# Kernel tuning notes

Hardware: AMD Instinct MI355X
Metric: run time of the kernel (lower is better)

## Reference

```python
import jax, jax.numpy as jnp
import numpy as np

D_MODEL = 1024
HEADS = 16
D_K = D_MODEL // HEADS
D_FF = 4096
EPS = 1e-5


def _layernorm(x, gamma, beta):
    mu = jnp.mean(x, axis=-1, keepdims=True)
    var = jnp.var(x, axis=-1, keepdims=True)
    return (x - mu) * jax.lax.rsqrt(var + EPS) * gamma + beta


def setup_inputs() -> dict:
    key = jax.random.key(0)
    ks = jax.random.split(key, 8)
    s = 0.02
    return {
        "x": jax.random.normal(ks[0], (4, 2048, D_MODEL), dtype=jnp.float32),
        "wq": jax.random.normal(ks[1], (D_MODEL, D_MODEL), dtype=jnp.float32) * s,
        "wk": jax.random.normal(ks[2], (D_MODEL, D_MODEL), dtype=jnp.float32) * s,
        "wv": jax.random.normal(ks[3], (D_MODEL, D_MODEL), dtype=jnp.float32) * s,
        "wo": jax.random.normal(ks[4], (D_MODEL, D_MODEL), dtype=jnp.float32) * s,
        "w1": jax.random.normal(ks[5], (D_MODEL, D_FF), dtype=jnp.float32) * s,
        "b1": jnp.zeros((D_FF,), dtype=jnp.float32),
        "w2": jax.random.normal(ks[6], (D_FF, D_MODEL), dtype=jnp.float32) * s,
        "b2": jnp.zeros((D_MODEL,), dtype=jnp.float32),
        "g1": jnp.ones((D_MODEL,), dtype=jnp.float32),
        "be1": jnp.zeros((D_MODEL,), dtype=jnp.float32),
        "g2": jnp.ones((D_MODEL,), dtype=jnp.float32),
        "be2": jnp.zeros((D_MODEL,), dtype=jnp.float32),
    }


def reference(x, wq, wk, wv, wo, w1, b1, w2, b2, g1, be1, g2, be2):
    B, S, D = x.shape
    # --- multi-head self-attention (dropout = identity at eval) ---
    q = (x @ wq).reshape(B, S, HEADS, D_K).transpose(0, 2, 1, 3)  # [B,H,S,dk]
    k = (x @ wk).reshape(B, S, HEADS, D_K).transpose(0, 2, 1, 3)
    v = (x @ wv).reshape(B, S, HEADS, D_K).transpose(0, 2, 1, 3)
    scores = jnp.einsum("bhqd,bhkd->bhqk", q, k) / jnp.sqrt(jnp.float32(D_K))
    attn = jax.nn.softmax(scores, axis=-1)
    ctx = jnp.einsum("bhqk,bhkd->bhqd", attn, v)
    ctx = ctx.transpose(0, 2, 1, 3).reshape(B, S, D)
    attn_out = ctx @ wo
    # --- add & norm 1 ---
    h = _layernorm(x + attn_out, g1, be1)
    # --- FFN ---
    ffn = jax.nn.relu(h @ w1 + b1) @ w2 + b2
    # --- add & norm 2 ---
    return _layernorm(h + ffn, g2, be2)
```

## Files before the change

### kernel.cpp

```cpp
#include <hip/hip_runtime.h>
#include <hip/hip_bf16.h>


typedef float  floatx2  __attribute__((ext_vector_type(2)));
typedef float  floatx4  __attribute__((ext_vector_type(4)));
typedef float  floatx16 __attribute__((ext_vector_type(16)));
typedef short  shortx8  __attribute__((ext_vector_type(8)));
typedef short  shortx4  __attribute__((ext_vector_type(4)));
typedef int    intx4    __attribute__((ext_vector_type(4)));
typedef unsigned uintx2 __attribute__((ext_vector_type(2)));

__device__ __forceinline__ short f2bs(float f) {
    union { float f; unsigned u; } a; a.f = f;
    unsigned r = a.u + 0x7fffu + ((a.u >> 16) & 1u);
    return (short)(r >> 16);
}

__device__ __forceinline__ float fexp2(float x) {
#if __has_builtin(__builtin_amdgcn_exp2f)
    return __builtin_amdgcn_exp2f(x);
#else
    return __expf(0.6931471805599453f * x);
#endif
}

__device__ __forceinline__ void lane32swap(unsigned& a, unsigned& b) {
#if __has_builtin(__builtin_amdgcn_permlane32_swap)
    uintx2 r = __builtin_amdgcn_permlane32_swap(a, b, false, false);
    a = r[0]; b = r[1];
#else
    int hl = (threadIdx.x & 63) >> 5;
    unsigned ta = (unsigned)__shfl_xor((int)a, 32);
    unsigned tb = (unsigned)__shfl_xor((int)b, 32);
    unsigned na = hl ? tb : a;
    unsigned nb = hl ? b : ta;
    a = na; b = nb;
#endif
}

__device__ __forceinline__ void gload16(const short* g, short* l) {
    __builtin_amdgcn_global_load_lds(
        (const __attribute__((address_space(1))) void*)g,
        (__attribute__((address_space(3))) void*)l,
        16, 0, 0);
}

#define WAITV(n) asm volatile("s_waitcnt vmcnt(" #n ")" ::: "memory")
#define FENCE    asm volatile("" ::: "memory")

__device__ __forceinline__ void trans_tile(const float* __restrict__ in,
                                           short* __restrict__ out,
                                           int N, int K, int k0, int n0,
                                           short (*t)[68]) {
    const int tid = threadIdx.x;
    const int r = tid >> 4, c4 = (tid & 15) * 4;
#pragma unroll
    for (int i = 0; i < 4; ++i) {
        int k = r + i * 16;
        floatx4 v = *(const floatx4*)(in + (size_t)(k0 + k) * N + n0 + c4);
        shortx4 s;
#pragma unroll
        for (int j = 0; j < 4; ++j) s[j] = f2bs(v[j]);
        *(shortx4*)(&t[k][c4]) = s;
    }
    __syncthreads();
#pragma unroll
    for (int i = 0; i < 4; ++i) {
        int n = r + i * 16;
        shortx4 s;
#pragma unroll
        for (int j = 0; j < 4; ++j) s[j] = t[c4 + j][n];
        *(shortx4*)(out + (size_t)(n0 + n) * K + k0 + c4) = s;
    }
}

__global__ __launch_bounds__(256) void prep_kernel(
    const float* __restrict__ wq, const float* __restrict__ wk,
    const float* __restrict__ wv, const float* __restrict__ wo,
    const float* __restrict__ w1, const float* __restrict__ w2,
    const float* __restrict__ x,
    short* wqt, short* wkt, short* wvt, short* wot,
    short* w1t, short* w2t, short* xb)
{
    __shared__ __align__(16) short t[64][68];
    const int bid = blockIdx.x;
    if (bid < 1024) {
        const int widx = bid >> 8, local = bid & 255;
        const float* in = widx == 0 ? wq : widx == 1 ? wk : widx == 2 ? wv : wo;
        short* out = widx == 0 ? wqt : widx == 1 ? wkt : widx == 2 ? wvt : wot;
        trans_tile(in, out, 1024, 1024, (local & 15) * 64, (local >> 4) * 64, t);
    } else if (bid < 2048) {
        const int local = bid - 1024;
        trans_tile(w1, w1t, 4096, 1024, (local & 15) * 64, (local >> 4) * 64, t);
    } else if (bid < 3072) {
        const int local = bid - 2048;
        trans_tile(w2, w2t, 1024, 4096, (local & 63) * 64, (local >> 6) * 64, t);
    } else {
        const int local = bid - 3072;
#pragma unroll
        for (int j = 0; j < 4; ++j) {
            int i = local * 1024 + j * 256 + threadIdx.x;
            floatx4 v = *(const floatx4*)(x + (size_t)i * 4);
            shortx4 o;
            o[0] = f2bs(v[0]); o[1] = f2bs(v[1]); o[2] = f2bs(v[2]); o[3] = f2bs(v[3]);
            *(shortx4*)(xb + (size_t)i * 4) = o;
        }
    }
}

template<int EPI, int BN>
__global__ __launch_bounds__(512, 2) void gemm256(
    const short* __restrict__ A, const short* __restrict__ Bt, const int K, const int N,
    short* __restrict__ outb, float* __restrict__ outf,
    const float* __restrict__ bias, const float* __restrict__ resf)
{
    constexpr int BUFSZ = 16384 + BN * 64;
    constexpr int NF = BN / 64;
    constexpr int NBUF = (BN == 128) ? 3 : 2;
    __shared__ __align__(16) short Ls[NBUF * BUFSZ];
    const int tid = threadIdx.x;
    const int w = tid >> 6, lane = tid & 63;
    const int quad = lane >> 4, l16 = lane & 15;
    const int wm = w >> 2, wn = w & 3;
    const int hsw = blockIdx.x + blockIdx.y * gridDim.x;
    const int vv = hsw >> 3;
    const int by = (hsw & 7) * 4 + (vv & 3);
    const int bx = vv >> 2;

    const int srow = w * 16 + (lane >> 3);
    const int uc0 = ((lane & 7) ^ ((lane >> 4) & 7)) * 8;
    const int uc1 = ((lane & 7) ^ (((lane >> 4) + 4) & 7)) * 8;
    const short* aS0 = A  + (size_t)(by * 256 + srow) * K + uc0;
    const short* aS1 = A  + (size_t)(by * 256 + srow + 8) * K + uc1;
    const short* bS0 = Bt + (size_t)(bx * BN + srow) * K + uc0;
    const short* bS1 = Bt + (size_t)(bx * BN + srow + 8) * K + uc1;
    const size_t hK = (size_t)128 * K;
    const int wsl = w * 1024;

    const int rswz = (l16 >> 1) & 7;
    const int ru0 = (quad ^ rswz) * 8;
    const int ru1 = ((4 + quad) ^ rswz) * 8;
    const int aRd = (wm * 64 + l16) * 64;
    const int bRd = (wn * 32 + l16) * 64;

    floatx4 acc[8][NF] = {};
    shortx8 af[4][2], blo[2][2], bhi[2][2];

#define S_A0(buf, kc) { short* p = Ls + (buf) * BUFSZ + wsl;         gload16(aS0 + (kc), p);      gload16(aS1 + (kc), p + 512);      FENCE; }
#define S_A1(buf, kc) { short* p = Ls + (buf) * BUFSZ + 8192 + wsl;  gload16(aS0 + hK + (kc), p); gload16(aS1 + hK + (kc), p + 512); FENCE; }
#define S_B0(buf, kc) { short* p = Ls + (buf) * BUFSZ + 16384 + wsl; gload16(bS0 + (kc), p);      gload16(bS1 + (kc), p + 512);      FENCE; }
#define S_B1(buf, kc) { short* p = Ls + (buf) * BUFSZ + 24576 + wsl; gload16(bS0 + hK + (kc), p); gload16(bS1 + hK + (kc), p + 512); FENCE; }
#define MF(a, b, c) c = __builtin_amdgcn_mfma_f32_16x16x32_bf16(a, b, c, 0, 0, 0)

#define RD_ALO(Ab) {                                                      \
_Pragma("unroll")                                                         \
        for (int mf = 0; mf < 4; ++mf) {                                  \
            af[mf][0] = *(const shortx8*)((Ab) + aRd + mf * 1024 + ru0);  \
            af[mf][1] = *(const shortx8*)((Ab) + aRd + mf * 1024 + ru1);  \
        } }
#define RD_AHI(Ab) {                                                      \
_Pragma("unroll")                                                         \
        for (int mf = 0; mf < 4; ++mf) {                                  \
            af[mf][0] = *(const shortx8*)((Ab) + aRd + 8192 + mf * 1024 + ru0); \
            af[mf][1] = *(const shortx8*)((Ab) + aRd + 8192 + mf * 1024 + ru1); \
        } }
#define RD_BLO(Bb) {                                                      \
_Pragma("unroll")                                                         \
        for (int nf = 0; nf < 2; ++nf) {                                  \
            blo[nf][0] = *(const shortx8*)((Bb) + bRd + nf * 1024 + ru0); \
            blo[nf][1] = *(const shortx8*)((Bb) + bRd + nf * 1024 + ru1); \
        } }
#define MFMA_LO { __builtin_amdgcn_s_setprio(1);                          \
_Pragma("unroll")                                                         \
        for (int mf = 0; mf < 4; ++mf)                                    \
_Pragma("unroll")                                                         \
            for (int nf = 0; nf < 2; ++nf) {                              \
                MF(af[mf][0], blo[nf][0], acc[mf][nf]);                   \
                MF(af[mf][1], blo[nf][1], acc[mf][nf]);                   \
            }                                                             \
        __builtin_amdgcn_s_setprio(0); }
#define MFMA_HI { __builtin_amdgcn_s_setprio(1);                          \
_Pragma("unroll")                                                         \
        for (int mf = 0; mf < 4; ++mf)                                    \
_Pragma("unroll")                                                         \
            for (int nf = 0; nf < 2; ++nf) {                              \
                MF(af[mf][0], blo[nf][0], acc[4 + mf][nf]);               \
                MF(af[mf][1], blo[nf][1], acc[4 + mf][nf]);               \
            }                                                             \
        __builtin_amdgcn_s_setprio(0); }

    const int NT = K >> 6;

    if constexpr (BN == 256) {
        S_A0(0, 0) S_B0(0, 0) S_B1(0, 0) S_A1(0, 0)
        for (int t = 0; t < NT - 1; ++t) {
            const int rb = t & 1, wbuf = rb ^ 1, kc = (t + 1) * 64;
            const short* Ab = Ls + rb * BUFSZ;
            const short* Bb = Ab + 16384;
            WAITV(4); __builtin_amdgcn_s_barrier(); FENCE;
            RD_ALO(Ab) RD_BLO(Bb)
            S_A0(wbuf, kc)
            MFMA_LO
            WAITV(4); __builtin_amdgcn_s_barrier(); FENCE;
#pragma unroll
            for (int nf = 0; nf < 2; ++nf) {
                bhi[nf][0] = *(const shortx8*)(Bb + bRd + 8192 + nf * 1024 + ru0);
                bhi[nf][1] = *(const shortx8*)(Bb + bRd + 8192 + nf * 1024 + ru1);
            }
            S_B0(wbuf, kc)
            __builtin_amdgcn_s_setprio(1);
#pragma unroll
            for (int mf = 0; mf < 4; ++mf)
#pragma unroll
                for (int nf = 0; nf < 2; ++nf) {
                    MF(af[mf][0], bhi[nf][0], acc[mf][2 + nf]);
                    MF(af[mf][1], bhi[nf][1], acc[mf][2 + nf]);
                }
            __builtin_amdgcn_s_setprio(0);
            WAITV(4); __builtin_amdgcn_s_barrier(); FENCE;
            RD_AHI(Ab)
            S_B1(wbuf, kc)
            MFMA_HI
            S_A1(wbuf, kc)
            __builtin_amdgcn_s_setprio(1);
#pragma unroll
            for (int mf = 0; mf < 4; ++mf)
#pragma unroll
                for (int nf = 0; nf < 2; ++nf) {
                    MF(af[mf][0], bhi[nf][0], acc[4 + mf][2 + nf]);
                    MF(af[mf][1], bhi[nf][1], acc[4 + mf][2 + nf]);
                }
            __builtin_amdgcn_s_setprio(0);
        }
        {
            const int rb = (NT - 1) & 1;
            const short* Ab = Ls + rb * BUFSZ;
            const short* Bb = Ab + 16384;
            WAITV(4); __builtin_amdgcn_s_barrier(); FENCE;
            RD_ALO(Ab) RD_BLO(Bb)
            MFMA_LO
            WAITV(2); __builtin_amdgcn_s_barrier(); FENCE;
#pragma unroll
            for (int nf = 0; nf < 2; ++nf) {
                bhi[nf][0] = *(const shortx8*)(Bb + bRd + 8192 + nf * 1024 + ru0);
                bhi[nf][1] = *(const shortx8*)(Bb + bRd + 8192 + nf * 1024 + ru1);
            }
            __builtin_amdgcn_s_setprio(1);
#pragma unroll
            for (int mf = 0; mf < 4; ++mf)
#pragma unroll
                for (int nf = 0; nf < 2; ++nf) {
                    MF(af[mf][0], bhi[nf][0], acc[mf][2 + nf]);
                    MF(af[mf][1], bhi[nf][1], acc[mf][2 + nf]);
                }
            __builtin_amdgcn_s_setprio(0);
            WAITV(0); __builtin_amdgcn_s_barrier(); FENCE;
            RD_AHI(Ab)
            __builtin_amdgcn_s_setprio(1);
#pragma unroll
            for (int mf = 0; mf < 4; ++mf)
#pragma unroll
                for (int nf = 0; nf < 2; ++nf) {
                    MF(af[mf][0], blo[nf][0], acc[4 + mf][nf]);
                    MF(af[mf][1], blo[nf][1], acc[4 + mf][nf]);
                    MF(af[mf][0], bhi[nf][0], acc[4 + mf][2 + nf]);
                    MF(af[mf][1], bhi[nf][1], acc[4 + mf][2 + nf]);
                }
            __builtin_amdgcn_s_setprio(0);
        }
    } else {
        S_A0(0, 0) S_B0(0, 0) S_A1(0, 0)
        S_A0(1, 64) S_B0(1, 64) S_A1(1, 64)
        for (int t = 0; t < NT - 2; ++t) {
            const int rb = t % 3, pb = (t + 2) % 3, kc = (t + 2) * 64;
            const short* Ab = Ls + rb * BUFSZ;
            const short* Bb = Ab + 16384;
            WAITV(8); __builtin_amdgcn_s_barrier(); FENCE;
            RD_ALO(Ab) RD_BLO(Bb)
            S_A0(pb, kc)
            MFMA_LO
            WAITV(8); __builtin_amdgcn_s_barrier(); FENCE;
            RD_AHI(Ab)
            S_B0(pb, kc) S_A1(pb, kc)
            MFMA_HI
        }
        {
            const int rb = (NT - 2) % 3;
            const short* Ab = Ls + rb * BUFSZ;
            const short* Bb = Ab + 16384;
            WAITV(8); __builtin_amdgcn_s_barrier(); FENCE;
            RD_ALO(Ab) RD_BLO(Bb)
            MFMA_LO
            WAITV(6); __builtin_amdgcn_s_barrier(); FENCE;
            RD_AHI(Ab)
            MFMA_HI
        }
        {
            const int rb = (NT - 1) % 3;
            const short* Ab = Ls + rb * BUFSZ;
            const short* Bb = Ab + 16384;
            WAITV(2); __builtin_amdgcn_s_barrier(); FENCE;
            RD_ALO(Ab) RD_BLO(Bb)
            MFMA_LO
            WAITV(0); __builtin_amdgcn_s_barrier(); FENCE;
            RD_AHI(Ab)
            MFMA_HI
        }
    }

#pragma unroll
    for (int mf = 0; mf < 8; ++mf) {
        const int grow0 = by * 256 + (mf >> 2) * 128 + wm * 64 + (mf & 3) * 16 + quad * 4;
#pragma unroll
        for (int nf = 0; nf < NF; ++nf) {
            int gcol;
            if constexpr (BN == 256)
                gcol = bx * 256 + (nf >> 1) * 128 + wn * 32 + (nf & 1) * 16 + l16;
            else
                gcol = bx * 128 + wn * 32 + nf * 16 + l16;
            const floatx4 a = acc[mf][nf];
            if constexpr (EPI == 5) {
                const int slice = gcol >> 10, c = gcol & 1023;
                const int hh = c >> 6, d = c & 63;
                const int b = grow0 >> 11, s0 = grow0 & 2047;
                if (slice == 2) {
                    short* vt = outb + ((size_t)16 << 20);
                    shortx4 pkv;
#pragma unroll
                    for (int r = 0; r < 4; ++r) pkv[r] = f2bs(a[r]);
                    *(shortx4*)(vt + ((size_t)((b * 16 + hh) * 64 + d)) * 2048 + s0) = pkv;
                } else {
                    short* dst = slice ? (outb + ((size_t)8 << 20)) : outb;
                    float sc = slice ? 1.f : 0.125f * 1.4426950408889634f;
#pragma unroll
                    for (int r = 0; r < 4; ++r)
                        dst[(((size_t)(b * 16 + hh)) * 2048 + (s0 + r)) * 64 + d] =
                            f2bs(a[r] * sc);
                }
            } else if constexpr (EPI == 1) {
                const float bv = bias[gcol];
#pragma unroll
                for (int r = 0; r < 4; ++r) {
                    float v = fmaxf(a[r] + bv, 0.f);
                    outb[(size_t)(grow0 + r) * N + gcol] = f2bs(v);
                }
            } else if constexpr (EPI == 2) {
#pragma unroll
                for (int r = 0; r < 4; ++r)
                    outf[(size_t)(grow0 + r) * N + gcol] =
                        a[r] + resf[(size_t)(grow0 + r) * N + gcol];
            } else if constexpr (EPI == 3) {
                const float bv = bias[gcol];
#pragma unroll
                for (int r = 0; r < 4; ++r)
                    outf[(size_t)(grow0 + r) * N + gcol] =
                        a[r] + bv + resf[(size_t)(grow0 + r) * N + gcol];
            }
        }
    }
#undef S_A0
#undef S_A1
#undef S_B0
#undef S_B1
#undef MF
#undef RD_ALO
#undef RD_AHI
#undef RD_BLO
#undef MFMA_LO
#undef MFMA_HI
}

__global__ __launch_bounds__(256) void ln_kernel(
    const float* __restrict__ in, float* __restrict__ outf, short* __restrict__ outb,
    const float* __restrict__ g, const float* __restrict__ be, int writeB)
{
    __shared__ float red[8];
    const int row = blockIdx.x, tid = threadIdx.x;
    const float* p = in + (size_t)row * 1024;
    floatx4 v = *(const floatx4*)(p + tid * 4);
    float s = v[0] + v[1] + v[2] + v[3];
    float q = v[0] * v[0] + v[1] * v[1] + v[2] * v[2] + v[3] * v[3];
#pragma unroll
    for (int off = 32; off; off >>= 1) {
        s += __shfl_xor(s, off);
        q += __shfl_xor(q, off);
    }
    int w = tid >> 6, lane = tid & 63;
    if (lane == 0) { red[w] = s; red[4 + w] = q; }
    __syncthreads();
    s = red[0] + red[1] + red[2] + red[3];
    q = red[4] + red[5] + red[6] + red[7];
    float mean = s * (1.f / 1024.f);
    float var = q * (1.f / 1024.f) - mean * mean;
    float rs = rsqrtf(var + 1e-5f);
    floatx4 gv = *(const floatx4*)(g + tid * 4);
    floatx4 bv = *(const floatx4*)(be + tid * 4);
    floatx4 o4;
#pragma unroll
    for (int i = 0; i < 4; ++i) o4[i] = (v[i] - mean) * rs * gv[i] + bv[i];
    *(floatx4*)(outf + (size_t)row * 1024 + tid * 4) = o4;
    if (writeB) {
        shortx4 ob;
#pragma unroll
        for (int i = 0; i < 4; ++i) ob[i] = f2bs(o4[i]);
        *(shortx4*)(outb + (size_t)row * 1024 + tid * 4) = ob;
    }
}

__global__ __launch_bounds__(256, 2) void attn_kernel(
    const short* __restrict__ Q, const short* __restrict__ K,
    const short* __restrict__ Vt, short* __restrict__ ctx)
{
    __shared__ __align__(16) short Ls[18432];
    const int tid = threadIdx.x;
    const int q0 = blockIdx.x * 256, bh = blockIdx.y;
    const int w = tid >> 6, lane = tid & 63, l31 = lane & 31, hl = lane >> 5;
    const size_t sb = (size_t)bh * 2048 * 64;

    shortx8 qf[2][4];
#pragma unroll
    for (int qg = 0; qg < 2; ++qg)
#pragma unroll
        for (int ks = 0; ks < 4; ++ks)
            qf[qg][ks] = *(const shortx8*)(Q + sb + (size_t)(q0 + w * 64 + qg * 32 + l31) * 64 + ks * 16 + hl * 8);

    const int srow = w * 8 + (lane >> 3);
    const int sunit = ((lane & 7) ^ (lane >> 3)) * 8;
    const short* kSrc = K + sb + (size_t)srow * 64 + sunit;
    const short* vSrc = Vt + sb + (size_t)srow * 2048 + sunit;
    const int sdst = w * 512;

    const int kx = l31 & 7;

    floatx16 o[2][2] = {};
    floatx2 rs0A = {0.f, 0.f}, rs0B = {0.f, 0.f};
    floatx2 rs1A = {0.f, 0.f}, rs1B = {0.f, 0.f};
    const floatx16 z = {};

#define STAGE(buf, kv0) { \
    short* kb = Ls + (buf) * 8192 + sdst; \
    gload16(kSrc + (size_t)(kv0) * 64, kb); \
    gload16(kSrc + (size_t)(kv0) * 64 + 2048, kb + 2048); \
    gload16(vSrc + (kv0), kb + 4096); \
    gload16(vSrc + (kv0) + 65536, kb + 6144); \
    FENCE; }

#define LD_AK(B, mt, ks) (*(const shortx8*)((B) + ((mt) * 32 + l31) * 64 + ((((ks) * 2 + hl) ^ kx)) * 8))
#define LD_AV(B, mtd, mt, ksl) (*(const shortx8*)((B) + 4096 + ((mtd) * 32 + l31) * 64 + ((((mt) * 4 + (ksl) * 2 + hl) ^ kx)) * 8))
#define MFA(a, b, c) __builtin_amdgcn_mfma_f32_32x32x16_bf16(a, b, c, 0, 0, 0)

    STAGE(0, 0)

    for (int kt = 0; kt < 32; ++kt) {
        WAITV(0);
        __builtin_amdgcn_s_barrier();
        FENCE;
        if (kt < 31) STAGE((kt + 1) & 1, (kt + 1) * 64)
        const short* B = Ls + (kt & 1) * 8192;

#pragma unroll
        for (int mt = 0; mt < 2; ++mt) {
            shortx8 ak[4], av[2][2];
#pragma unroll
            for (int ks = 0; ks < 4; ++ks) ak[ks] = LD_AK(B, mt, ks);
#pragma unroll
            for (int ksl = 0; ksl < 2; ++ksl)
#pragma unroll
                for (int mtd = 0; mtd < 2; ++mtd) av[ksl][mtd] = LD_AV(B, mtd, mt, ksl);
            floatx16 sc0, sc1;
            __builtin_amdgcn_s_setprio(1);
            sc0 = MFA(ak[0], qf[0][0], z);
            sc0 = MFA(ak[1], qf[0][1], sc0);
            sc0 = MFA(ak[2], qf[0][2], sc0);
            sc0 = MFA(ak[3], qf[0][3], sc0);
            sc1 = MFA(ak[0], qf[1][0], z);
            sc1 = MFA(ak[1], qf[1][1], sc1);
            sc1 = MFA(ak[2], qf[1][2], sc1);
            sc1 = MFA(ak[3], qf[1][3], sc1);
            __builtin_amdgcn_s_setprio(0);
#pragma unroll
            for (int qg = 0; qg < 2; ++qg) {
                const floatx16 sc = qg ? sc1 : sc0;
                floatx2 ps2[8];
#pragma unroll
                for (int i = 0; i < 8; ++i) {
                    ps2[i][0] = fexp2(sc[2 * i]);
                    ps2[i][1] = fexp2(sc[2 * i + 1]);
                }
                if (qg == 0) {
#pragma unroll
                    for (int i = 0; i < 8; i += 2) { rs0A += ps2[i]; rs0B += ps2[i + 1]; }
                } else {
#pragma unroll
                    for (int i = 0; i < 8; i += 2) { rs1A += ps2[i]; rs1B += ps2[i + 1]; }
                }
                unsigned pk[8];
#pragma unroll
                for (int i = 0; i < 8; ++i) {
                    union { __hip_bfloat162 h; unsigned u; } cv;
                    cv.h = __float22bfloat162_rn(make_float2(ps2[i][0], ps2[i][1]));
                    pk[i] = cv.u;
                }
                lane32swap(pk[0], pk[2]);
                lane32swap(pk[1], pk[3]);
                lane32swap(pk[4], pk[6]);
                lane32swap(pk[5], pk[7]);
                __builtin_amdgcn_s_setprio(1);
#pragma unroll
                for (int ksl = 0; ksl < 2; ++ksl) {
                    union { unsigned i[4]; shortx8 s8; } fr;
                    fr.i[0] = pk[4 * ksl];     fr.i[1] = pk[4 * ksl + 1];
                    fr.i[2] = pk[4 * ksl + 2]; fr.i[3] = pk[4 * ksl + 3];
#pragma unroll
                    for (int mtd = 0; mtd < 2; ++mtd)
                        o[qg][mtd] = MFA(av[ksl][mtd], fr.s8, o[qg][mtd]);
                }
                __builtin_amdgcn_s_setprio(0);
            }
        }
    }
#undef STAGE
#undef LD_AK
#undef LD_AV
#undef MFA

    float inv0, inv1;
    {
        float r0 = rs0A[0] + rs0A[1] + rs0B[0] + rs0B[1];
        float t0 = r0 + __shfl_xor(r0, 32);
        inv0 = 1.f / t0;
        float r1 = rs1A[0] + rs1A[1] + rs1B[0] + rs1B[1];
        float t1 = r1 + __shfl_xor(r1, 32);
        inv1 = 1.f / t1;
    }

    __syncthreads();
    short* O_lds = Ls;
#pragma unroll
    for (int qg = 0; qg < 2; ++qg) {
        const float inv = qg ? inv1 : inv0;
#pragma unroll
        for (int mtd = 0; mtd < 2; ++mtd)
#pragma unroll
            for (int g = 0; g < 4; ++g) {
                shortx4 p4;
#pragma unroll
                for (int r = 0; r < 4; ++r) p4[r] = f2bs(o[qg][mtd][4 * g + r] * inv);
                *(shortx4*)(O_lds + (w * 64 + qg * 32 + l31) * 72 + mtd * 32 + g * 8 + hl * 4) = p4;
            }
    }
    __syncthreads();
    const int b = bh >> 4, head = bh & 15;
#pragma unroll
    for (int it = 0; it < 8; ++it) {
        int idx = it * 256 + tid;
        int q = idx >> 3, ch = idx & 7;
        shortx8 v = *(const shortx8*)(O_lds + q * 72 + ch * 8);
        *(shortx8*)(ctx + ((size_t)(b * 2048 + q0 + q)) * 1024 + head * 64 + ch * 8) = v;
    }
}

extern "C" void kernel_launch(void* const* d_in, const int* in_sizes, int n_in,
                              void* d_out, int out_size, void* d_ws, size_t ws_size,
                              hipStream_t stream) {
    const float* x   = (const float*)d_in[0];
    const float* wq  = (const float*)d_in[1];
    const float* wk  = (const float*)d_in[2];
    const float* wv  = (const float*)d_in[3];
    const float* wo  = (const float*)d_in[4];
    const float* w1  = (const float*)d_in[5];
    const float* b1  = (const float*)d_in[6];
    const float* w2  = (const float*)d_in[7];
    const float* b2  = (const float*)d_in[8];
    const float* g1p = (const float*)d_in[9];
    const float* be1 = (const float*)d_in[10];
    const float* g2p = (const float*)d_in[11];
    const float* be2 = (const float*)d_in[12];
    float* out = (float*)d_out;

    char* ws = (char*)d_ws;
    const size_t MB = 1ull << 20;
    short* wqt  = (short*)(ws + 0 * MB);
    short* wkt  = (short*)(ws + 2 * MB);
    short* wvt  = (short*)(ws + 4 * MB);
    short* wot  = (short*)(ws + 6 * MB);
    short* w1t  = (short*)(ws + 8 * MB);
    short* w2t  = (short*)(ws + 16 * MB);
    short* xb   = (short*)(ws + 24 * MB);
    short* Qb   = (short*)(ws + 40 * MB);
    short* Kb   = (short*)(ws + 56 * MB);
    short* Vtg  = (short*)(ws + 72 * MB);
    short* ctxb = (short*)(ws + 88 * MB);
    float* tf   = (float*)(ws + 104 * MB);
    short* hb   = (short*)(ws + 136 * MB);
    short* f1b  = (short*)(ws + 40 * MB);

    prep_kernel<<<5120, 256, 0, stream>>>(wq, wk, wv, wo, w1, w2, x,
                                          wqt, wkt, wvt, wot, w1t, w2t, xb);

    gemm256<5, 128><<<dim3(24, 32), 512, 0, stream>>>(xb, wqt, 1024, 3072, Qb, nullptr, nullptr, nullptr);
    attn_kernel<<<dim3(8, 64), 256, 0, stream>>>(Qb, Kb, Vtg, ctxb);
    gemm256<2, 128><<<dim3(8, 32), 512, 0, stream>>>(ctxb, wot, 1024, 1024, nullptr, tf, nullptr, x);
    ln_kernel<<<8192, 256, 0, stream>>>(tf, tf, hb, g1p, be1, 1);
    gemm256<1, 256><<<dim3(16, 32), 512, 0, stream>>>(hb, w1t, 1024, 4096, f1b, nullptr, b1, nullptr);
    gemm256<3, 128><<<dim3(8, 32), 512, 0, stream>>>(f1b, w2t, 4096, 1024, nullptr, out, b2, tf);
    ln_kernel<<<8192, 256, 0, stream>>>(out, out, nullptr, g2p, be2, 0);
}
```

Before: 356.3 us.

## Split attention KV range across two blocks and merge partials in a combine kernel

The attention kernel now handles only half of the key/value sequence per block, which doubles the grid to 1024 blocks and raises the launch-bounds occupancy hint to 4 blocks per CU. Each block writes its unnormalized bf16 partial output and its per-row exp-sum to workspace. A new combine kernel adds the two partials, divides by the total sum, and writes ctx in the head-interleaved layout. The aim is more parallelism and better latency hiding in attention. In exchange it adds extra global traffic, one more launch, bf16 rounding of the unnormalized partials, and possible register pressure or spills under the tighter launch bound.

```diff
diff --git a/kernel.cpp b/kernel.cpp
--- a/kernel.cpp
+++ b/kernel.cpp
@@ -407,15 +407,19 @@
     }
 }
 
-__global__ __launch_bounds__(256, 2) void attn_kernel(
+__global__ __launch_bounds__(256, 4) void attn_kernel(
     const short* __restrict__ Q, const short* __restrict__ K,
-    const short* __restrict__ Vt, short* __restrict__ ctx)
+    const short* __restrict__ Vt, short* __restrict__ oPA,
+    short* __restrict__ oPB, float* __restrict__ rsP)
 {
     __shared__ __align__(16) short Ls[18432];
     const int tid = threadIdx.x;
-    const int q0 = blockIdx.x * 256, bh = blockIdx.y;
+    const int bh = blockIdx.x;
+    const int qt = blockIdx.y >> 1, kvh = blockIdx.y & 1;
+    const int q0 = qt * 256;
     const int w = tid >> 6, lane = tid & 63, l31 = lane & 31, hl = lane >> 5;
     const size_t sb = (size_t)bh * 2048 * 64;
+    const int kvbase = kvh * 1024;
 
     shortx8 qf[2][4];
 #pragma unroll
@@ -449,13 +453,13 @@
 #define LD_AV(B, mtd, mt, ksl) (*(const shortx8*)((B) + 4096 + ((mtd) * 32 + l31) * 64 + ((((mt) * 4 + (ksl) * 2 + hl) ^ kx)) * 8))
 #define MFA(a, b, c) __builtin_amdgcn_mfma_f32_32x32x16_bf16(a, b, c, 0, 0, 0)
 
-    STAGE(0, 0)
-
-    for (int kt = 0; kt < 32; ++kt) {
+    STAGE(0, kvbase)
+
+    for (int kt = 0; kt < 16; ++kt) {
         WAITV(0);
         __builtin_amdgcn_s_barrier();
         FENCE;
-        if (kt < 31) STAGE((kt + 1) & 1, (kt + 1) * 64)
+        if (kt < 15) STAGE((kt + 1) & 1, kvbase + (kt + 1) * 64)
         const short* B = Ls + (kt & 1) * 8192;
 
 #pragma unroll
@@ -524,40 +528,64 @@
 #undef LD_AV
 #undef MFA
 
-    float inv0, inv1;
+    float t0, t1;
     {
         float r0 = rs0A[0] + rs0A[1] + rs0B[0] + rs0B[1];
-        float t0 = r0 + __shfl_xor(r0, 32);
-        inv0 = 1.f / t0;
+        t0 = r0 + __shfl_xor(r0, 32);
         float r1 = rs1A[0] + rs1A[1] + rs1B[0] + rs1B[1];
-        float t1 = r1 + __shfl_xor(r1, 32);
-        inv1 = 1.f / t1;
-    }
-
+        t1 = r1 + __shfl_xor(r1, 32);
+    }
+    if (hl == 0) {
+        float* rp = rsP + (size_t)kvh * 131072 + bh * 2048 + q0;
+        rp[w * 64 + l31] = t0;
+        rp[w * 64 + 32 + l31] = t1;
+    }
+
+    short* oP = kvh ? oPB : oPA;
     __syncthreads();
     short* O_lds = Ls;
 #pragma unroll
     for (int qg = 0; qg < 2; ++qg) {
-        const float inv = qg ? inv1 : inv0;
 #pragma unroll
         for (int mtd = 0; mtd < 2; ++mtd)
 #pragma unroll
             for (int g = 0; g < 4; ++g) {
                 shortx4 p4;
 #pragma unroll
-                for (int r = 0; r < 4; ++r) p4[r] = f2bs(o[qg][mtd][4 * g + r] * inv);
+                for (int r = 0; r < 4; ++r) p4[r] = f2bs(o[qg][mtd][4 * g + r]);
                 *(shortx4*)(O_lds + (w * 64 + qg * 32 + l31) * 72 + mtd * 32 + g * 8 + hl * 4) = p4;
             }
     }
     __syncthreads();
-    const int b = bh >> 4, head = bh & 15;
 #pragma unroll
     for (int it = 0; it < 8; ++it) {
         int idx = it * 256 + tid;
         int q = idx >> 3, ch = idx & 7;
         shortx8 v = *(const shortx8*)(O_lds + q * 72 + ch * 8);
-        *(shortx8*)(ctx + ((size_t)(b * 2048 + q0 + q)) * 1024 + head * 64 + ch * 8) = v;
-    }
+        *(shortx8*)(oP + sb + (size_t)(q0 + q) * 64 + ch * 8) = v;
+    }
+}
+
+__global__ __launch_bounds__(256) void combine_kernel(
+    const short* __restrict__ oPA, const short* __restrict__ oPB,
+    const float* __restrict__ rsP, short* __restrict__ ctx)
+{
+    const int gid = blockIdx.x * 256 + threadIdx.x;
+    const int row = gid >> 3, dg = (gid & 7) * 8;
+    const int bh = row >> 11, q = row & 2047;
+    const float inv = 1.f / (rsP[row] + rsP[131072 + row]);
+    shortx8 a = *(const shortx8*)(oPA + (size_t)row * 64 + dg);
+    shortx8 b = *(const shortx8*)(oPB + (size_t)row * 64 + dg);
+    shortx8 o;
+#pragma unroll
+    for (int i = 0; i < 8; ++i) {
+        union { unsigned u; float f; } fa, fb;
+        fa.u = ((unsigned)(unsigned short)a[i]) << 16;
+        fb.u = ((unsigned)(unsigned short)b[i]) << 16;
+        o[i] = f2bs((fa.f + fb.f) * inv);
+    }
+    const int bb = bh >> 4, head = bh & 15;
+    *(shortx8*)(ctx + ((size_t)(bb * 2048 + q)) * 1024 + head * 64 + dg) = o;
 }
 
 extern "C" void kernel_launch(void* const* d_in, const int* in_sizes, int n_in,
@@ -594,12 +622,16 @@
     float* tf   = (float*)(ws + 104 * MB);
     short* hb   = (short*)(ws + 136 * MB);
     short* f1b  = (short*)(ws + 40 * MB);
+    short* oPA  = (short*)(ws + 24 * MB);
+    short* oPB  = (short*)(ws + 104 * MB);
+    float* rsP  = (float*)(ws + 120 * MB);
 
     prep_kernel<<<5120, 256, 0, stream>>>(wq, wk, wv, wo, w1, w2, x,
                                           wqt, wkt, wvt, wot, w1t, w2t, xb);
 
     gemm256<5, 128><<<dim3(24, 32), 512, 0, stream>>>(xb, wqt, 1024, 3072, Qb, nullptr, nullptr, nullptr);
-    attn_kernel<<<dim3(8, 64), 256, 0, stream>>>(Qb, Kb, Vtg, ctxb);
+    attn_kernel<<<dim3(64, 16), 256, 0, stream>>>(Qb, Kb, Vtg, oPA, oPB, rsP);
+    combine_kernel<<<4096, 256, 0, stream>>>(oPA, oPB, rsP, ctxb);
     gemm256<2, 128><<<dim3(8, 32), 512, 0, stream>>>(ctxb, wot, 1024, 1024, nullptr, tf, nullptr, x);
     ln_kernel<<<8192, 256, 0, stream>>>(tf, tf, hb, g1p, be1, 1);
     gemm256<1, 256><<<dim3(16, 32), 512, 0, stream>>>(hb, w1t, 1024, 4096, f1b, nullptr, b1, nullptr);
```

New measurement: 692.0 us. 1.94x slower.
